# Optimization experiments

Measured on AMD Instinct MI355X. Metric: run time of the kernel, lower is better.

Reference implementation:

```python
import jax, jax.numpy as jnp
import numpy as np

BLOCK_SIZE = 32
FP6_E2M3_MAX = 7.5

def _build_fp6_e2m3_grid():
    vals = set()
    for bits in range(64):
        s = (bits >> 5) & 1
        e = (bits >> 3) & 3
        m = bits & 7
        v = (m / 8.0) if e == 0 else (1.0 + m / 8.0) * 2.0 ** (e - 1)
        vals.add(-v if s else v)
    return np.array(sorted(vals), dtype=np.float32)

_GRID = jnp.asarray(_build_fp6_e2m3_grid())  # sorted 1-D fp32 grid (46 unique values)

def _nearest_on_grid(x, grid):
    # round-to-nearest on a sorted grid via searchsorted (matches torch reference)
    idx = jnp.clip(jnp.searchsorted(grid, x), 0, grid.shape[0] - 1)
    idx_lo = jnp.maximum(idx - 1, 0)
    v_hi = grid[idx]
    v_lo = grid[idx_lo]
    return jnp.where(jnp.abs(x - v_lo) <= jnp.abs(x - v_hi), v_lo, v_hi)

def _mx_quantize(t, eps=1e-30):
    # t: (rows, K) fp32, K divisible by BLOCK_SIZE
    rows, K = t.shape
    blocks = t.reshape(rows, K // BLOCK_SIZE, BLOCK_SIZE)
    scales = jnp.maximum(jnp.max(jnp.abs(blocks), axis=-1) / FP6_E2M3_MAX, eps)  # (rows, nb)
    q = _nearest_on_grid(blocks / scales[..., None], _GRID)  # fp6-simulated fp32
    return q, scales

def setup_inputs() -> dict:
    key = jax.random.key(0)
    k1, k2, k3 = jax.random.split(key, 3)
    x = jax.random.normal(k1, (8, 8192, 1024), dtype=jnp.float32)
    weight = jax.random.normal(k2, (1024, 1024), dtype=jnp.float32) * 0.02
    bias = jax.random.normal(k3, (1024,), dtype=jnp.float32) * 0.02
    return {"x": x, "weight": weight, "bias": bias}

def reference(x, weight, bias):
    batch_shape = x.shape[:-1]
    in_features = x.shape[-1]
    x2 = x.astype(jnp.float32).reshape(-1, in_features)      # (N, K)
    w2 = weight.astype(jnp.float32)                           # (J, K)
    xq, xs = _mx_quantize(x2)                                 # (N, nb, bs), (N, nb)
    wq, ws = _mx_quantize(w2)                                 # (J, nb, bs), (J, nb)
    # out[n, j] = sum_b xs[n,b] * ws[j,b] * dot(xq[n,b,:], wq[j,b,:])
    # == dequant(x) @ dequant(w).T  (fold fp32 scales into quantized blocks)
    xd = (xq * xs[..., None]).reshape(x2.shape)
    wd = (wq * ws[..., None]).reshape(w2.shape)
    out = xd @ wd.T + bias
    return out.reshape(*batch_shape, -1)
```

## Files before the change

### kernel.cpp

```cpp
#include <hip/hip_runtime.h>
#include <stdint.h>

#define K_DIM 1024
#define N_DIM 1024
#define M_DIM 65536

typedef __bf16 bf16_t;
typedef __bf16 bf16x8 __attribute__((ext_vector_type(8)));
typedef float f32x4 __attribute__((ext_vector_type(4)));

#define GLOAD_LDS16(g, l) __builtin_amdgcn_global_load_lds( \
    (const __attribute__((address_space(1))) void*)(g),     \
    (__attribute__((address_space(3))) void*)(l), 16, 0, 0)

#define VMCNT(n) asm volatile("s_waitcnt vmcnt(%0)" ::"n"(n) : "memory")

__global__ __launch_bounds__(256) void quant_dequant_kernel(
    const float* __restrict__ in, bf16_t* __restrict__ out, long long nvec) {
  long long i = (long long)blockIdx.x * blockDim.x + threadIdx.x;
  long long stride = (long long)gridDim.x * blockDim.x;
  for (; i < nvec; i += stride) {
    long long base = i * 8;
    f32x4 v0 = *reinterpret_cast<const f32x4*>(in + base);
    f32x4 v1 = *reinterpret_cast<const f32x4*>(in + base + 4);
    float mx = 0.0f;
#pragma unroll
    for (int j = 0; j < 4; ++j) {
      mx = fmaxf(mx, fabsf(v0[j]));
      mx = fmaxf(mx, fabsf(v1[j]));
    }
    mx = fmaxf(mx, __shfl_xor(mx, 1));
    mx = fmaxf(mx, __shfl_xor(mx, 2));
    float s = fmaxf(mx / 7.5f, 1e-30f);
    bf16x8 o;
#pragma unroll
    for (int j = 0; j < 8; ++j) {
      float xv = (j < 4) ? v0[j] : v1[j - 4];
      float y = xv / s;
      float m = fabsf(y);
      float h, hinv;
      if (m < 2.0f)      { h = 0.125f; hinv = 8.0f; }
      else if (m < 4.0f) { h = 0.25f;  hinv = 4.0f; }
      else               { h = 0.5f;   hinv = 2.0f; }
      float n = m * hinv;
      float kf = floorf(n);
      float fr = n - kf;
      float up = (fr > 0.5f || (fr == 0.5f && y < 0.0f)) ? 1.0f : 0.0f;
      float q = fminf((kf + up) * h, 7.5f);
      o[j] = (bf16_t)(copysignf(q, y) * s);
    }
    *reinterpret_cast<bf16x8*>(out + base) = o;
  }
}

__global__ __launch_bounds__(512, 2) void mx_gemm(
    const bf16_t* __restrict__ A, const bf16_t* __restrict__ B,
    const float* __restrict__ bias, float* __restrict__ C) {
  __shared__ char lds[131072];

  const int tid = threadIdx.x;
  const int lane = tid & 63;
  const int wid = tid >> 6;
  const int wm = wid >> 2;
  const int wn = wid & 3;

  const int b = blockIdx.x;
  const int xcd = b & 7;
  const int t = b >> 3;
  const int m_tile = xcd * 32 + (t >> 2);
  const int n_tile = t & 3;

  const int R0 = tid >> 2;
  const int c0 = ((tid & 3) ^ ((tid >> 2) & 3)) * 8;
  const bf16_t* aS0 = A + (size_t)(m_tile * 256 + R0) * K_DIM + c0;
  const bf16_t* aS1 = aS0 + (size_t)128 * K_DIM;
  const bf16_t* bS0 = B + (size_t)(n_tile * 256 + R0) * K_DIM + c0;
  const bf16_t* bS1 = bS0 + (size_t)128 * K_DIM;
  const int dstOff = wid * 1024 + lane * 16;

  auto STAGE = [&](int u) {
    char* sbase = lds + (u & 3) * 32768;
    const int ko = u * 32;
    GLOAD_LDS16(aS0 + ko, sbase + dstOff);
    GLOAD_LDS16(aS1 + ko, sbase + 8192 + dstOff);
    GLOAD_LDS16(bS0 + ko, sbase + 16384 + dstOff);
    GLOAD_LDS16(bS1 + ko, sbase + 24576 + dstOff);
  };

  const int ps = (((lane >> 4) ^ (lane & 3)) << 4);
  const int rowb = (lane & 15) * 64 + ps;
  const int aOff = wm * 8192 + rowb;
  const int bOff = 16384 + wn * 4096 + rowb;

  f32x4 acc[8][4];
#pragma unroll
  for (int i = 0; i < 8; ++i)
#pragma unroll
    for (int j = 0; j < 4; ++j) acc[i][j] = (f32x4)(0.0f);

  auto COMPUTE = [&](int u) {
    const char* sbase = lds + (u & 3) * 32768;
    bf16x8 bf[4], af[4];
#pragma unroll
    for (int j = 0; j < 4; ++j)
      bf[j] = *reinterpret_cast<const bf16x8*>(sbase + bOff + j * 1024);
#pragma unroll
    for (int i = 0; i < 4; ++i)
      af[i] = *reinterpret_cast<const bf16x8*>(sbase + aOff + i * 1024);
    __builtin_amdgcn_s_setprio(1);
#pragma unroll
    for (int i = 0; i < 4; ++i)
#pragma unroll
      for (int j = 0; j < 4; ++j)
        acc[i][j] = __builtin_amdgcn_mfma_f32_16x16x32_bf16(af[i], bf[j],
                                                            acc[i][j], 0, 0, 0);
    __builtin_amdgcn_s_setprio(0);
#pragma unroll
    for (int i = 0; i < 4; ++i)
      af[i] = *reinterpret_cast<const bf16x8*>(sbase + aOff + 4096 + i * 1024);
    __builtin_amdgcn_s_setprio(1);
#pragma unroll
    for (int i = 0; i < 4; ++i)
#pragma unroll
      for (int j = 0; j < 4; ++j)
        acc[4 + i][j] = __builtin_amdgcn_mfma_f32_16x16x32_bf16(
            af[i], bf[j], acc[4 + i][j], 0, 0, 0);
    __builtin_amdgcn_s_setprio(0);
  };

  STAGE(0);
  STAGE(1);
  STAGE(2);

  for (int kt = 0; kt < 29; ++kt) {
    VMCNT(8);
    __builtin_amdgcn_s_barrier();
    __builtin_amdgcn_sched_barrier(0);
    STAGE(kt + 3);
    COMPUTE(kt);
  }
  VMCNT(8);
  __builtin_amdgcn_s_barrier();
  __builtin_amdgcn_sched_barrier(0);
  COMPUTE(29);
  VMCNT(4);
  __builtin_amdgcn_s_barrier();
  __builtin_amdgcn_sched_barrier(0);
  COMPUTE(30);
  VMCNT(0);
  __builtin_amdgcn_s_barrier();
  __builtin_amdgcn_sched_barrier(0);
  COMPUTE(31);

  const int col0 = n_tile * 256 + wn * 64 + (lane & 15);
  const int row0 = m_tile * 256 + wm * 128 + ((lane >> 4) << 2);
#pragma unroll
  for (int j = 0; j < 4; ++j) {
    float bv = bias[col0 + j * 16];
#pragma unroll
    for (int m = 0; m < 8; ++m) {
#pragma unroll
      for (int r = 0; r < 4; ++r) {
        C[(size_t)(row0 + m * 16 + r) * N_DIM + col0 + j * 16] =
            acc[m][j][r] + bv;
      }
    }
  }
}

extern "C" void kernel_launch(void* const* d_in, const int* in_sizes, int n_in,
                              void* d_out, int out_size, void* d_ws,
                              size_t ws_size, hipStream_t stream) {
  const float* x = (const float*)d_in[0];
  const float* w = (const float*)d_in[1];
  const float* bias = (const float*)d_in[2];
  float* out = (float*)d_out;

  bf16_t* xd = (bf16_t*)d_ws;
  bf16_t* wd = xd + (size_t)M_DIM * K_DIM;

  quant_dequant_kernel<<<4096, 256, 0, stream>>>(x, xd,
                                                 (long long)M_DIM * K_DIM / 8);
  quant_dequant_kernel<<<512, 256, 0, stream>>>(w, wd,
                                                (long long)K_DIM * N_DIM / 8);

  mx_gemm<<<(M_DIM / 256) * (N_DIM / 256), 512, 0, stream>>>(xd, wd, bias,
                                                             out);
}
```

Before: 273.6 us.

## Software-pipeline LDS fragment loads across k-steps and change LDS swizzle

Splits each k-step into two phases so the B and first-half A fragments for the next stage are read from LDS right after the barrier, overlapping those reads with the MFMAs on the current stage. Fragments are double-buffered in registers (bfA/bfB, afA/afB) and the loop is unrolled by two, with explicit lgkmcnt waits. The LDS staging layout and read swizzle are also changed (XOR on different row bits, linear tid destination), aiming to cut bank conflicts. This raises register pressure under a 2-waves-per-SIMD launch bound and adds fragile manual wait-count bookkeeping.

After: 269.8 us. About the same (-1.4%).

```diff
diff --git a/kernel.cpp b/kernel.cpp
--- a/kernel.cpp
+++ b/kernel.cpp
@@ -14,6 +14,8 @@
     (__attribute__((address_space(3))) void*)(l), 16, 0, 0)
 
 #define VMCNT(n) asm volatile("s_waitcnt vmcnt(%0)" ::"n"(n) : "memory")
+#define LGKM(n) asm volatile("s_waitcnt lgkmcnt(%0)" ::"n"(n) : "memory")
+#define SCHEDB() __builtin_amdgcn_sched_barrier(0)
 
 __global__ __launch_bounds__(256) void quant_dequant_kernel(
     const float* __restrict__ in, bf16_t* __restrict__ out, long long nvec) {
@@ -71,23 +73,24 @@
   const int n_tile = t & 3;
 
   const int R0 = tid >> 2;
-  const int c0 = ((tid & 3) ^ ((tid >> 2) & 3)) * 8;
+  const int c0 = ((tid & 3) ^ ((tid >> 3) & 3)) * 8;
   const bf16_t* aS0 = A + (size_t)(m_tile * 256 + R0) * K_DIM + c0;
   const bf16_t* aS1 = aS0 + (size_t)128 * K_DIM;
   const bf16_t* bS0 = B + (size_t)(n_tile * 256 + R0) * K_DIM + c0;
   const bf16_t* bS1 = bS0 + (size_t)128 * K_DIM;
-  const int dstOff = wid * 1024 + lane * 16;
-
-  auto STAGE = [&](int u) {
-    char* sbase = lds + (u & 3) * 32768;
-    const int ko = u * 32;
-    GLOAD_LDS16(aS0 + ko, sbase + dstOff);
-    GLOAD_LDS16(aS1 + ko, sbase + 8192 + dstOff);
-    GLOAD_LDS16(bS0 + ko, sbase + 16384 + dstOff);
-    GLOAD_LDS16(bS1 + ko, sbase + 24576 + dstOff);
-  };
-
-  const int ps = (((lane >> 4) ^ (lane & 3)) << 4);
+  const int dstOff = tid * 16;
+
+#define STAGE(u)                                         \
+  {                                                      \
+    char* sb_ = lds + ((u) & 3) * 32768;                 \
+    const int ko_ = (u) * 32;                            \
+    GLOAD_LDS16(aS0 + ko_, sb_ + dstOff);                \
+    GLOAD_LDS16(aS1 + ko_, sb_ + 8192 + dstOff);         \
+    GLOAD_LDS16(bS0 + ko_, sb_ + 16384 + dstOff);        \
+    GLOAD_LDS16(bS1 + ko_, sb_ + 24576 + dstOff);        \
+  }
+
+  const int ps = (((lane >> 4) ^ ((lane >> 1) & 3)) << 4);
   const int rowb = (lane & 15) * 64 + ps;
   const int aOff = wm * 8192 + rowb;
   const int bOff = 16384 + wn * 4096 + rowb;
@@ -98,59 +101,80 @@
 #pragma unroll
     for (int j = 0; j < 4; ++j) acc[i][j] = (f32x4)(0.0f);
 
-  auto COMPUTE = [&](int u) {
-    const char* sbase = lds + (u & 3) * 32768;
-    bf16x8 bf[4], af[4];
-#pragma unroll
-    for (int j = 0; j < 4; ++j)
-      bf[j] = *reinterpret_cast<const bf16x8*>(sbase + bOff + j * 1024);
-#pragma unroll
-    for (int i = 0; i < 4; ++i)
-      af[i] = *reinterpret_cast<const bf16x8*>(sbase + aOff + i * 1024);
-    __builtin_amdgcn_s_setprio(1);
-#pragma unroll
-    for (int i = 0; i < 4; ++i)
-#pragma unroll
-      for (int j = 0; j < 4; ++j)
-        acc[i][j] = __builtin_amdgcn_mfma_f32_16x16x32_bf16(af[i], bf[j],
-                                                            acc[i][j], 0, 0, 0);
-    __builtin_amdgcn_s_setprio(0);
-#pragma unroll
-    for (int i = 0; i < 4; ++i)
-      af[i] = *reinterpret_cast<const bf16x8*>(sbase + aOff + 4096 + i * 1024);
-    __builtin_amdgcn_s_setprio(1);
-#pragma unroll
-    for (int i = 0; i < 4; ++i)
-#pragma unroll
-      for (int j = 0; j < 4; ++j)
-        acc[4 + i][j] = __builtin_amdgcn_mfma_f32_16x16x32_bf16(
-            af[i], bf[j], acc[4 + i][j], 0, 0, 0);
-    __builtin_amdgcn_s_setprio(0);
-  };
+  bf16x8 bfA[4], bfB[4], afA[4], afB[4], af1[4];
+
+#define PH_A(T, BF, AF0, DO_STG)                                          \
+  {                                                                       \
+    const char* sb_ = lds + ((T) & 3) * 32768;                            \
+    _Pragma("unroll") for (int i = 0; i < 4; ++i) af1[i] =                \
+        *reinterpret_cast<const bf16x8*>(sb_ + aOff + 4096 + i * 1024);   \
+    if (DO_STG) STAGE((T) + 3);                                           \
+    LGKM(4);                                                              \
+    SCHEDB();                                                             \
+    __builtin_amdgcn_s_setprio(1);                                        \
+    _Pragma("unroll") for (int i = 0; i < 4; ++i)                         \
+        _Pragma("unroll") for (int j = 0; j < 4; ++j) acc[i][j] =         \
+            __builtin_amdgcn_mfma_f32_16x16x32_bf16(AF0[i], BF[j],        \
+                                                    acc[i][j], 0, 0, 0);  \
+    __builtin_amdgcn_s_setprio(0);                                        \
+  }
+
+#define PH_B(T, BF, NBF, NAF0, VMN, DO_PRE)                                  \
+  {                                                                          \
+    VMCNT(VMN);                                                              \
+    LGKM(0);                                                                 \
+    __builtin_amdgcn_s_barrier();                                            \
+    SCHEDB();                                                                \
+    if (DO_PRE) {                                                            \
+      const char* sn_ = lds + (((T) + 1) & 3) * 32768;                       \
+      _Pragma("unroll") for (int j = 0; j < 4; ++j) NBF[j] =                 \
+          *reinterpret_cast<const bf16x8*>(sn_ + bOff + j * 1024);           \
+      _Pragma("unroll") for (int i = 0; i < 4; ++i) NAF0[i] =                \
+          *reinterpret_cast<const bf16x8*>(sn_ + aOff + i * 1024);           \
+    }                                                                        \
+    __builtin_amdgcn_s_setprio(1);                                           \
+    _Pragma("unroll") for (int i = 0; i < 4; ++i)                            \
+        _Pragma("unroll") for (int j = 0; j < 4; ++j) acc[4 + i][j] =        \
+            __builtin_amdgcn_mfma_f32_16x16x32_bf16(af1[i], BF[j],           \
+                                                    acc[4 + i][j], 0, 0, 0); \
+    __builtin_amdgcn_s_setprio(0);                                           \
+  }
 
   STAGE(0);
   STAGE(1);
   STAGE(2);
-
-  for (int kt = 0; kt < 29; ++kt) {
-    VMCNT(8);
-    __builtin_amdgcn_s_barrier();
-    __builtin_amdgcn_sched_barrier(0);
-    STAGE(kt + 3);
-    COMPUTE(kt);
-  }
   VMCNT(8);
   __builtin_amdgcn_s_barrier();
-  __builtin_amdgcn_sched_barrier(0);
-  COMPUTE(29);
-  VMCNT(4);
-  __builtin_amdgcn_s_barrier();
-  __builtin_amdgcn_sched_barrier(0);
-  COMPUTE(30);
-  VMCNT(0);
-  __builtin_amdgcn_s_barrier();
-  __builtin_amdgcn_sched_barrier(0);
-  COMPUTE(31);
+  SCHEDB();
+#pragma unroll
+  for (int j = 0; j < 4; ++j)
+    bfA[j] = *reinterpret_cast<const bf16x8*>(lds + bOff + j * 1024);
+#pragma unroll
+  for (int i = 0; i < 4; ++i)
+    afA[i] = *reinterpret_cast<const bf16x8*>(lds + aOff + i * 1024);
+
+  for (int p = 0; p < 14; ++p) {
+    const int u = 2 * p;
+    PH_A(u, bfA, afA, true);
+    PH_B(u, bfA, bfB, afB, 8, true);
+    PH_A(u + 1, bfB, afB, true);
+    PH_B(u + 1, bfB, bfA, afA, 8, true);
+  }
+  PH_A(28, bfA, afA, true);
+  PH_B(28, bfA, bfB, afB, 8, true);
+  PH_A(29, bfB, afB, false);
+  PH_B(29, bfB, bfA, afA, 4, true);
+  PH_A(30, bfA, afA, false);
+  PH_B(30, bfA, bfB, afB, 0, true);
+  PH_A(31, bfB, afB, false);
+  LGKM(0);
+  SCHEDB();
+#pragma unroll
+  for (int i = 0; i < 4; ++i)
+#pragma unroll
+    for (int j = 0; j < 4; ++j)
+      acc[4 + i][j] = __builtin_amdgcn_mfma_f32_16x16x32_bf16(
+          af1[i], bfB[j], acc[4 + i][j], 0, 0, 0);
 
   const int col0 = n_tile * 256 + wn * 64 + (lane & 15);
   const int row0 = m_tile * 256 + wm * 128 + ((lane >> 4) << 2);
@@ -166,6 +190,9 @@
       }
     }
   }
+#undef STAGE
+#undef PH_A
+#undef PH_B
 }
 
 extern "C" void kernel_launch(void* const* d_in, const int* in_sizes, int n_in,
```
